# Kernel tuning notes

Measured on AMD Instinct MI355X. Metric: run time of the kernel, lower is better.

The kernel has to match this reference:

```python
import jax, jax.numpy as jnp
import numpy as np

NB_CLASSES = 10
NB_NEIGHBORS = 75  # 1 closest + 74 precomputed geodesic neighbors


def setup_inputs() -> dict:
    key = jax.random.key(0)
    k0, k1, k2, k3, k4, k5 = jax.random.split(key, 6)
    nb_data, nb_train, d = 1024, 100000, 256
    x = jax.random.normal(k0, (nb_data, d), dtype=jnp.float32)
    X = jax.random.normal(k1, (nb_train, d), dtype=jnp.float32)
    # train table is stored normalized + centered (init_nn_querier)
    X = X / jnp.linalg.norm(X, axis=1, keepdims=True)
    X = X - jnp.mean(X, axis=0)
    center = jax.random.normal(k2, (d,), dtype=jnp.float32) * 0.01
    train_labels = jax.random.randint(k3, (nb_train,), 0, NB_CLASSES).astype(jnp.int32)
    train_neighbor_index = jax.random.randint(
        k4, (nb_train, NB_NEIGHBORS - 1), 0, nb_train).astype(jnp.int32)
    cali_nonconformity = jnp.sort(
        jax.random.randint(k5, (1000,), 0, NB_NEIGHBORS)).astype(jnp.int32)
    return {
        "x": x, "X": X, "center": center,
        "train_labels": train_labels,
        "train_neighbor_index": train_neighbor_index,
        "cali_nonconformity": cali_nonconformity,
    }


def reference(x, X, center, train_labels, train_neighbor_index, cali_nonconformity):
    # --- find_train_knns: normalize query, center, closest-neighbor search ---
    xq = x / jnp.linalg.norm(x, axis=1, keepdims=True) - center  # [B, d]
    # squared euclidean distances to every train point: [B, nb_train]
    d2 = (jnp.sum(xq * xq, axis=1, keepdims=True)
          - 2.0 * (xq @ X.T)
          + jnp.sum(X * X, axis=1)[None, :])
    closest = jnp.argmin(d2, axis=1)                               # [B]
    # neighbor list = closest point prepended to its precomputed table row
    neigh = jnp.concatenate(
        [closest[:, None], train_neighbor_index[closest]], axis=1)  # [B, K]
    knns_labels = train_labels[neigh]                              # [B, K]
    # --- nonconformity: per-class bincount, #knns NOT in class ---
    counts = jnp.sum(jax.nn.one_hot(knns_labels, NB_CLASSES, dtype=jnp.int32),
                     axis=1)                                       # [B, C]
    knns_not_in_class = jnp.sum(counts, axis=1, keepdims=True) - counts
    # --- preds_conf_cred: conformal p-values via bisect_left ---
    nb_cali = cali_nonconformity.shape[0]
    pos = jnp.searchsorted(cali_nonconformity, knns_not_in_class, side='left')
    p_value = (nb_cali - pos).astype(jnp.float32) / float(nb_cali)  # [B, C]
    preds = jnp.argmax(p_value, axis=1)                             # [B]
    top2, _ = jax.lax.top_k(p_value, 2)                             # [B, 2]
    nb_data = p_value.shape[0]
    creds = jnp.zeros_like(p_value).at[jnp.arange(nb_data), preds].set(top2[:, 0])
    return creds
```

## Files before the change

kernel.cpp:

```cpp
#include <hip/hip_runtime.h>
#include <stdint.h>


typedef __attribute__((ext_vector_type(8))) short short8;
typedef __attribute__((ext_vector_type(4))) float float4v;

static __device__ __forceinline__ unsigned short bf16_rn(float f) {
    unsigned int u = __float_as_uint(f);
    unsigned int r = (u + 0x7FFFu + ((u >> 16) & 1u)) >> 16;
    return (unsigned short)r;
}

static __device__ __forceinline__ void gload_lds16(const void* g, void* l) {
    __builtin_amdgcn_global_load_lds(
        (const __attribute__((address_space(1))) unsigned int*)g,
        (__attribute__((address_space(3))) unsigned int*)l, 16, 0, 0);
}

__global__ __launch_bounds__(256) void prep_q(
    const float* __restrict__ x, const float* __restrict__ center,
    unsigned short* __restrict__ Ah, float* __restrict__ xqf,
    float* __restrict__ q2a, float* __restrict__ al2q, int B, int Mp)
{
    const int tid = threadIdx.x;
    const int row = blockIdx.x;
    __shared__ float p1[4], p2[4], p3[4];
    if (row >= Mp) return;
    if (row >= B) {
        Ah[(size_t)row * 256 + tid] = 0;
        xqf[(size_t)row * 256 + tid] = 0.f;
        if (tid == 0) { q2a[row] = 0.f; al2q[row] = 0.f; }
        return;
    }
    float v = x[(size_t)row * 256 + tid];
    float ss = v * v;
    #pragma unroll
    for (int s = 1; s < 64; s <<= 1) ss += __shfl_xor(ss, s);
    if ((tid & 63) == 0) p1[tid >> 6] = ss;
    __syncthreads();
    float tot = p1[0] + p1[1] + p1[2] + p1[3];
    float inv = 1.0f / sqrtf(tot);
    float val = v * inv - center[tid];
    unsigned short hb = bf16_rn(val);
    float hf = __uint_as_float((unsigned int)hb << 16);
    float al = val - hf;
    Ah[(size_t)row * 256 + tid] = hb;
    xqf[(size_t)row * 256 + tid] = val;
    float ss2 = val * val, sal = al * al;
    #pragma unroll
    for (int s = 1; s < 64; s <<= 1) {
        ss2 += __shfl_xor(ss2, s);
        sal += __shfl_xor(sal, s);
    }
    if ((tid & 63) == 0) { p2[tid >> 6] = ss2; p3[tid >> 6] = sal; }
    __syncthreads();
    if (tid == 0) {
        q2a[row]  = p2[0] + p2[1] + p2[2] + p2[3];
        al2q[row] = p3[0] + p3[1] + p3[2] + p3[3];
    }
}

__global__ __launch_bounds__(256, 4) void mfma_tile(
    const unsigned short* __restrict__ Ah,
    const float* __restrict__ X,
    float* __restrict__ xn2,
    float* __restrict__ pmax,
    float* __restrict__ gmin,
    int Mp, int Np, int nb_train, int B,
    int ntiles, int nper, int mtiles)
{
    __shared__ unsigned short As[128 * 64];
    __shared__ unsigned short Bs[128 * 64];
    __shared__ float xnl[128];
    __shared__ float sm4[4];

    const int bid = blockIdx.x;
    const int xcd = bid & 7;
    const int s_  = bid >> 3;
    const int n_t = xcd * nper + (s_ / mtiles);
    const int m_t = s_ - (s_ / mtiles) * mtiles;
    if (n_t >= ntiles) return;
    const int mtile = m_t * 128;
    const int ntile = n_t * 128;

    const int tid  = threadIdx.x;
    const int wave = tid >> 6;
    const int lane = tid & 63;

    const int Rwave  = (wave & 1) * 64;
    const int lrow8  = lane >> 3;
    const int lchunk = lane & 7;
    const unsigned short* sbaseA =
        Ah + (size_t)(mtile + Rwave + lrow8) * 256 + (size_t)((lchunk ^ lrow8) * 8);
    unsigned short* lwaveA = As + Rwave * 64;

    const int brow = tid >> 1;
    const int bh   = tid & 1;
    const bool bok = (ntile + brow) < nb_train;
    const float* bsrc = X + (size_t)(ntile + brow) * 256 + bh * 32;
    const int bsw = brow & 7;
    unsigned short* brp = Bs + brow * 64;
    float bss = 0.f;

    const int mq = (wave >> 1) * 64;
    const int nq = (wave & 1) * 64;
    const int lrow = lane & 15;
    const int kseg = lane >> 4;
    const int sw = lrow & 7;

    float4v acc[4][4];
    #pragma unroll
    for (int i = 0; i < 4; ++i)
        #pragma unroll
        for (int j = 0; j < 4; ++j)
            acc[i][j] = (float4v){0.f, 0.f, 0.f, 0.f};

    for (int s = 0; s < 4; ++s) {
        __syncthreads();
        if (wave < 2) {
            const unsigned short* g = sbaseA + (size_t)(s * 64);
            #pragma unroll
            for (int q = 0; q < 8; ++q)
                gload_lds16(g + q * 2048, lwaveA + q * 512);
        }
        const float* srcs = bsrc + s * 64;
        #pragma unroll
        for (int hb = 0; hb < 2; ++hb) {
            short8 c0, c1;
            if (bok) {
                const float4* sp = (const float4*)(srcs + hb * 16);
                float4 f0 = sp[0], f1 = sp[1], f2 = sp[2], f3 = sp[3];
                c0[0] = (short)bf16_rn(f0.x); c0[1] = (short)bf16_rn(f0.y);
                c0[2] = (short)bf16_rn(f0.z); c0[3] = (short)bf16_rn(f0.w);
                c0[4] = (short)bf16_rn(f1.x); c0[5] = (short)bf16_rn(f1.y);
                c0[6] = (short)bf16_rn(f1.z); c0[7] = (short)bf16_rn(f1.w);
                c1[0] = (short)bf16_rn(f2.x); c1[1] = (short)bf16_rn(f2.y);
                c1[2] = (short)bf16_rn(f2.z); c1[3] = (short)bf16_rn(f2.w);
                c1[4] = (short)bf16_rn(f3.x); c1[5] = (short)bf16_rn(f3.y);
                c1[6] = (short)bf16_rn(f3.z); c1[7] = (short)bf16_rn(f3.w);
                bss += f0.x * f0.x + f0.y * f0.y + f0.z * f0.z + f0.w * f0.w
                     + f1.x * f1.x + f1.y * f1.y + f1.z * f1.z + f1.w * f1.w
                     + f2.x * f2.x + f2.y * f2.y + f2.z * f2.z + f2.w * f2.w
                     + f3.x * f3.x + f3.y * f3.y + f3.z * f3.z + f3.w * f3.w;
            } else {
                c0 = (short8){0, 0, 0, 0, 0, 0, 0, 0};
                c1 = c0;
            }
            const int cA = bh * 4 + hb * 2;
            *(short8*)&brp[(cA ^ bsw) * 8]       = c0;
            *(short8*)&brp[((cA + 1) ^ bsw) * 8] = c1;
        }
        __syncthreads();
        #pragma unroll
        for (int t = 0; t < 2; ++t) {
            const int wch = ((t * 4 + kseg) ^ sw) * 8;
            short8 a[4], b[4];
            #pragma unroll
            for (int i = 0; i < 4; ++i)
                a[i] = *(const short8*)&As[(mq + i * 16 + lrow) * 64 + wch];
            #pragma unroll
            for (int j = 0; j < 4; ++j)
                b[j] = *(const short8*)&Bs[(nq + j * 16 + lrow) * 64 + wch];
            #pragma unroll
            for (int i = 0; i < 4; ++i)
                #pragma unroll
                for (int j = 0; j < 4; ++j)
                    acc[i][j] = __builtin_amdgcn_mfma_f32_16x16x32_bf16(
                        a[i], b[j], acc[i][j], 0, 0, 0);
        }
    }

    float stot = bss + __shfl_xor(bss, 1);
    if (bh == 0) xnl[brow] = bok ? stot : 3.0e38f;
    float mx = (bh == 0 && bok) ? stot : 0.f;
    #pragma unroll
    for (int sft = 1; sft < 64; sft <<= 1) mx = fmaxf(mx, __shfl_xor(mx, sft));
    if (lane == 0) sm4[wave] = mx;
    __syncthreads();
    if (m_t == 0) {
        if (tid < 128) xn2[ntile + tid] = xnl[tid];
        if (tid == 0)
            pmax[n_t] = fmaxf(fmaxf(sm4[0], sm4[1]), fmaxf(sm4[2], sm4[3]));
    }

    const int ng64 = Np >> 6;
    const int gb = (ntile + nq) >> 6;
    float xnv[4];
    #pragma unroll
    for (int j = 0; j < 4; ++j)
        xnv[j] = xnl[nq + j * 16 + lrow];

    #pragma unroll
    for (int i = 0; i < 4; ++i) {
        #pragma unroll
        for (int r = 0; r < 4; ++r) {
            const int lm = mq + i * 16 + kseg * 4 + r;
            const int gq = mtile + lm;
            float vm = fminf(
                fminf(xnv[0] - 2.0f * acc[i][0][r], xnv[1] - 2.0f * acc[i][1][r]),
                fminf(xnv[2] - 2.0f * acc[i][2][r], xnv[3] - 2.0f * acc[i][3][r]));
            #pragma unroll
            for (int sft = 1; sft < 16; sft <<= 1)
                vm = fminf(vm, __shfl_xor(vm, sft));
            if (lrow == 0 && gq < B)
                gmin[(size_t)gq * ng64 + gb] = vm;
        }
    }
}

__global__ __launch_bounds__(256) void select_classify(
    const float* __restrict__ gmin, const float* __restrict__ xqf,
    const float* __restrict__ X, const float* __restrict__ xn2,
    const float* __restrict__ q2a, const float* __restrict__ al2q,
    const float* __restrict__ pmax,
    const int* __restrict__ labels, const int* __restrict__ nbr,
    const int* __restrict__ cali, float* __restrict__ out,
    int Np, int nb_train, int knm1, int nb_cali, int B, int npm)
{
    extern __shared__ float gbuf[];
    __shared__ float xq_s[256];
    __shared__ float wmin[4], wpm[4], fsc[4];
    __shared__ int   fid[4];
    __shared__ float s_thr;
    __shared__ int   cand[256];
    __shared__ int   s_ncand;
    __shared__ int   s_closest;

    const int q    = blockIdx.x;
    const int tid  = threadIdx.x;
    const int lane = tid & 63;
    const int wave = tid >> 6;
    const int ng64 = Np >> 6;

    if (tid == 0) s_ncand = 0;
    xq_s[tid] = xqf[(size_t)q * 256 + tid];
    float vmin = 3.4e38f;
    for (int i = tid; i < ng64; i += 256) {
        float v = gmin[(size_t)q * ng64 + i];
        gbuf[i] = v;
        vmin = fminf(vmin, v);
    }
    float pm = 0.f;
    for (int i = tid; i < npm; i += 256) pm = fmaxf(pm, pmax[i]);
    #pragma unroll
    for (int s = 1; s < 64; s <<= 1) {
        vmin = fminf(vmin, __shfl_xor(vmin, s));
        pm   = fmaxf(pm,   __shfl_xor(pm, s));
    }
    if (lane == 0) { wmin[wave] = vmin; wpm[wave] = pm; }
    __syncthreads();
    if (tid == 0) {
        float m = fminf(fminf(wmin[0], wmin[1]), fminf(wmin[2], wmin[3]));
        float mb2 = fmaxf(fmaxf(wpm[0], wpm[1]), fmaxf(wpm[2], wpm[3]));
        float maxb  = sqrtf(mb2);
        float maxbl = maxb * 0.00390625f;
        float an = sqrtf(q2a[q]), al = sqrtf(al2q[q]);
        float errdot = al * maxb * 1.00390625f + (an + al) * maxbl;
        s_thr = m + 4.0f * errdot + 1e-3f;
    }
    __syncthreads();
    const float thr = s_thr;
    for (int g = tid; g < ng64; g += 256) {
        if (gbuf[g] <= thr) {
            int p = atomicAdd(&s_ncand, 1);
            if (p < 256) cand[p] = g;
        }
    }
    __syncthreads();
    const int nc = s_ncand;

    const int rsub = tid & 3;
    const int rrow = tid >> 2;
    float bsc = 3.4e38f; int bidx = 0x7FFFFFFF;
    auto rescore = [&](int g) {
        int row = g * 64 + rrow;
        if (row < nb_train) {
            const float* xr = X + (size_t)row * 256 + rsub * 64;
            const float* xs = xq_s + rsub * 64;
            float dot = 0.f;
            #pragma unroll
            for (int k = 0; k < 16; ++k) {
                float4 a4 = *(const float4*)(xs + k * 4);
                float4 b4 = *(const float4*)(xr + k * 4);
                dot += a4.x * b4.x + a4.y * b4.y + a4.z * b4.z + a4.w * b4.w;
            }
            dot += __shfl_xor(dot, 1);
            dot += __shfl_xor(dot, 2);
            float sc = xn2[row] - 2.0f * dot;
            if (sc < bsc || (sc == bsc && row < bidx)) { bsc = sc; bidx = row; }
        }
    };
    if (nc <= 256) {
        for (int c = 0; c < nc; ++c) rescore(cand[c]);
    } else {
        for (int g = 0; g < ng64; ++g)
            if (gbuf[g] <= thr) rescore(g);
    }
    #pragma unroll
    for (int s = 1; s < 64; s <<= 1) {
        float osc = __shfl_xor(bsc, s);
        int   oid = __shfl_xor(bidx, s);
        if (osc < bsc || (osc == bsc && oid < bidx)) { bsc = osc; bidx = oid; }
    }
    if (lane == 0) { fsc[wave] = bsc; fid[wave] = bidx; }
    __syncthreads();
    if (tid == 0) {
        float bs = fsc[0]; int bi = fid[0];
        #pragma unroll
        for (int w = 1; w < 4; ++w)
            if (fsc[w] < bs || (fsc[w] == bs && fid[w] < bi)) { bs = fsc[w]; bi = fid[w]; }
        s_closest = bi;
    }
    __syncthreads();

    if (wave == 0) {
        const int closest = s_closest;
        const int K = knm1 + 1;
        int lbl0 = -1, lbl1 = -1;
        if (lane < K) {
            int idx = (lane == 0) ? closest : nbr[(size_t)closest * knm1 + (lane - 1)];
            lbl0 = labels[idx];
        }
        int j2 = lane + 64;
        if (j2 < K) {
            int idx = nbr[(size_t)closest * knm1 + (j2 - 1)];
            lbl1 = labels[idx];
        }
        int bestc = 0, bestp = -1;
        #pragma unroll
        for (int c = 0; c < 10; ++c) {
            int cnt = __popcll(__ballot(lbl0 == c)) + __popcll(__ballot(lbl1 == c));
            int v = K - cnt;
            int lo = 0, hi = nb_cali;
            while (lo < hi) {
                int mid = (lo + hi) >> 1;
                if (cali[mid] < v) lo = mid + 1; else hi = mid;
            }
            int p = nb_cali - lo;
            if (p > bestp) { bestp = p; bestc = c; }
        }
        float pv = (float)bestp / (float)nb_cali;
        if (lane < 10)
            out[(size_t)q * 10 + lane] = (lane == bestc) ? pv : 0.0f;
    }
}

extern "C" void kernel_launch(void* const* d_in, const int* in_sizes, int n_in,
                              void* d_out, int out_size, void* d_ws, size_t ws_size,
                              hipStream_t stream) {
    const float* x      = (const float*)d_in[0];
    const float* X      = (const float*)d_in[1];
    const float* center = (const float*)d_in[2];
    const int* labels   = (const int*)d_in[3];
    const int* nbr      = (const int*)d_in[4];
    const int* cali     = (const int*)d_in[5];
    float* out = (float*)d_out;

    const int d        = in_sizes[2];
    const int B        = in_sizes[0] / d;
    const int nb_train = in_sizes[3];
    const int knm1     = in_sizes[4] / nb_train;
    const int nb_cali  = in_sizes[5];

    const int Mp = (B + 127) & ~127;
    const int Np = (nb_train + 127) & ~127;
    const int ng64 = Np >> 6;
    const int ntiles = Np / 128;
    const int mtiles = Mp / 128;
    const int nper   = (ntiles + 7) / 8;

    char* ws = (char*)d_ws;
    size_t off = 0;
    float* gmin = (float*)(ws + off);          off += (size_t)Mp * ng64 * 4;
    unsigned short* Ah = (unsigned short*)(ws + off); off += (size_t)Mp * 256 * 2;
    float* xqf  = (float*)(ws + off);          off += (size_t)Mp * 256 * 4;
    float* q2a  = (float*)(ws + off);          off += (size_t)Mp * 4;
    float* al2q = (float*)(ws + off);          off += (size_t)Mp * 4;
    float* xn2  = (float*)(ws + off);          off += (size_t)Np * 4;
    float* pmax = (float*)(ws + off);          off += (size_t)ntiles * 4;

    prep_q<<<Mp, 256, 0, stream>>>(x, center, Ah, xqf, q2a, al2q, B, Mp);

    mfma_tile<<<8 * nper * mtiles, 256, 0, stream>>>(
        Ah, X, xn2, pmax, gmin, Mp, Np, nb_train, B, ntiles, nper, mtiles);

    select_classify<<<B, 256, ng64 * 4, stream>>>(
        gmin, xqf, X, xn2, q2a, al2q, pmax, labels, nbr, cali, out,
        Np, nb_train, knm1, nb_cali, B, ntiles);
}
```

Before: 357.1 us.

## Prefetch next B k-slice into registers and coalesce X loads across lanes

The X tile is now loaded with 8 lanes covering one row's 64-float k-slice, each lane taking one 8-float chunk. This gives coalesced global reads instead of each thread streaming 32 contiguous floats. The next slice is register-prefetched during the current MFMA stage so global latency overlaps compute. Row norms are reduced by shuffles across the 8 lanes. The cost is higher register pressure (32 extra floats held live across the MFMA loop), which could hurt occupancy.

Result: slower. 901.1 us (+152.3%).

```diff
diff --git a/kernel.cpp b/kernel.cpp
--- a/kernel.cpp
+++ b/kernel.cpp
@@ -94,13 +94,29 @@
         Ah + (size_t)(mtile + Rwave + lrow8) * 256 + (size_t)((lchunk ^ lrow8) * 8);
     unsigned short* lwaveA = As + Rwave * 64;
 
-    const int brow = tid >> 1;
-    const int bh   = tid & 1;
-    const bool bok = (ntile + brow) < nb_train;
-    const float* bsrc = X + (size_t)(ntile + brow) * 256 + bh * 32;
-    const int bsw = brow & 7;
-    unsigned short* brp = Bs + brow * 64;
-    float bss = 0.f;
+    const int brow0  = wave * 32 + lrow8;
+    const int bchunk = lchunk ^ lrow8;
+    const size_t bsrcoff = (size_t)bchunk * 8;
+
+    float4 f[4][2];
+    bool   bok[4];
+    #pragma unroll
+    for (int j = 0; j < 4; ++j) bok[j] = (ntile + brow0 + j * 8) < nb_train;
+
+    auto loadB = [&](int s) {
+        #pragma unroll
+        for (int j = 0; j < 4; ++j) {
+            if (bok[j]) {
+                const float4* sp = (const float4*)(
+                    X + (size_t)(ntile + brow0 + j * 8) * 256 + s * 64 + bsrcoff);
+                f[j][0] = sp[0];
+                f[j][1] = sp[1];
+            } else {
+                f[j][0] = make_float4(0.f, 0.f, 0.f, 0.f);
+                f[j][1] = f[j][0];
+            }
+        }
+    };
 
     const int mq = (wave >> 1) * 64;
     const int nq = (wave & 1) * 64;
@@ -115,6 +131,10 @@
         for (int j = 0; j < 4; ++j)
             acc[i][j] = (float4v){0.f, 0.f, 0.f, 0.f};
 
+    float rowss[4] = {0.f, 0.f, 0.f, 0.f};
+
+    loadB(0);
+
     for (int s = 0; s < 4; ++s) {
         __syncthreads();
         if (wave < 2) {
@@ -123,33 +143,19 @@
             for (int q = 0; q < 8; ++q)
                 gload_lds16(g + q * 2048, lwaveA + q * 512);
         }
-        const float* srcs = bsrc + s * 64;
-        #pragma unroll
-        for (int hb = 0; hb < 2; ++hb) {
-            short8 c0, c1;
-            if (bok) {
-                const float4* sp = (const float4*)(srcs + hb * 16);
-                float4 f0 = sp[0], f1 = sp[1], f2 = sp[2], f3 = sp[3];
-                c0[0] = (short)bf16_rn(f0.x); c0[1] = (short)bf16_rn(f0.y);
-                c0[2] = (short)bf16_rn(f0.z); c0[3] = (short)bf16_rn(f0.w);
-                c0[4] = (short)bf16_rn(f1.x); c0[5] = (short)bf16_rn(f1.y);
-                c0[6] = (short)bf16_rn(f1.z); c0[7] = (short)bf16_rn(f1.w);
-                c1[0] = (short)bf16_rn(f2.x); c1[1] = (short)bf16_rn(f2.y);
-                c1[2] = (short)bf16_rn(f2.z); c1[3] = (short)bf16_rn(f2.w);
-                c1[4] = (short)bf16_rn(f3.x); c1[5] = (short)bf16_rn(f3.y);
-                c1[6] = (short)bf16_rn(f3.z); c1[7] = (short)bf16_rn(f3.w);
-                bss += f0.x * f0.x + f0.y * f0.y + f0.z * f0.z + f0.w * f0.w
-                     + f1.x * f1.x + f1.y * f1.y + f1.z * f1.z + f1.w * f1.w
-                     + f2.x * f2.x + f2.y * f2.y + f2.z * f2.z + f2.w * f2.w
-                     + f3.x * f3.x + f3.y * f3.y + f3.z * f3.z + f3.w * f3.w;
-            } else {
-                c0 = (short8){0, 0, 0, 0, 0, 0, 0, 0};
-                c1 = c0;
-            }
-            const int cA = bh * 4 + hb * 2;
-            *(short8*)&brp[(cA ^ bsw) * 8]       = c0;
-            *(short8*)&brp[((cA + 1) ^ bsw) * 8] = c1;
-        }
+        #pragma unroll
+        for (int j = 0; j < 4; ++j) {
+            float4 a = f[j][0], b = f[j][1];
+            short8 c;
+            c[0] = (short)bf16_rn(a.x); c[1] = (short)bf16_rn(a.y);
+            c[2] = (short)bf16_rn(a.z); c[3] = (short)bf16_rn(a.w);
+            c[4] = (short)bf16_rn(b.x); c[5] = (short)bf16_rn(b.y);
+            c[6] = (short)bf16_rn(b.z); c[7] = (short)bf16_rn(b.w);
+            *(short8*)&Bs[(brow0 + j * 8) * 64 + lchunk * 8] = c;
+            rowss[j] += a.x * a.x + a.y * a.y + a.z * a.z + a.w * a.w
+                      + b.x * b.x + b.y * b.y + b.z * b.z + b.w * b.w;
+        }
+        if (s + 1 < 4) loadB(s + 1);
         __syncthreads();
         #pragma unroll
         for (int t = 0; t < 2; ++t) {
@@ -170,9 +176,18 @@
         }
     }
 
-    float stot = bss + __shfl_xor(bss, 1);
-    if (bh == 0) xnl[brow] = bok ? stot : 3.0e38f;
-    float mx = (bh == 0 && bok) ? stot : 0.f;
+    float mx = 0.f;
+    #pragma unroll
+    for (int j = 0; j < 4; ++j) {
+        float v = rowss[j];
+        v += __shfl_xor(v, 1);
+        v += __shfl_xor(v, 2);
+        v += __shfl_xor(v, 4);
+        if ((lane & 7) == 0) {
+            xnl[brow0 + j * 8] = bok[j] ? v : 3.0e38f;
+            if (bok[j]) mx = fmaxf(mx, v);
+        }
+    }
     #pragma unroll
     for (int sft = 1; sft < 64; sft <<= 1) mx = fmaxf(mx, __shfl_xor(mx, sft));
     if (lane == 0) sm4[wave] = mx;
```
